# Optimization experiments

Measured on AMD Instinct MI355X. Metric: run time of the kernel, lower is better.

The kernel has to match this reference:

```python
import jax, jax.numpy as jnp
import numpy as np

N, D = 8192, 1024


def setup_inputs() -> dict:
    key = jax.random.key(0)
    k1, k2, k3 = jax.random.split(key, 3)
    f_1 = jax.random.normal(k1, (N, D), dtype=jnp.float32)
    f_2 = jax.random.normal(k2, (N, D), dtype=jnp.float32)
    f_3 = jax.random.normal(k3, (N, D), dtype=jnp.float32)
    return {"f_1": f_1, "f_2": f_2, "f_3": f_3, "batch": 3}


def _svdvals(x):
    # torch.svd computes full U, S, V; only singular values are consumed.
    return jnp.linalg.svd(x, compute_uv=False)


def reference(f_1, f_2, f_3, batch):
    if batch == 2:
        s_1 = _svdvals(f_1)
        if f_2.shape[0] == 0:
            return s_1[0] ** 2
        s_2 = _svdvals(f_2)
        return s_1.mean() + s_2.mean()
    elif batch == 3:
        s_1 = _svdvals(f_1)
        s_2 = _svdvals(f_2)
        s_3 = _svdvals(f_3)
        return s_1[0] ** 2 + 0.5 * (s_2[0] ** 2 + s_3[0] ** 2)
```

## Files before the change

### kernel.cpp

```cpp
#include <hip/hip_runtime.h>


#define DIM 1024
#define NROW 8192
#define MSZ (DIM*DIM)
#define NS 6

typedef __attribute__((ext_vector_type(8))) short short8;
typedef __attribute__((ext_vector_type(4))) float f32x4;

__device__ inline float bf2f(unsigned short u) {
    union { unsigned i; float f; } x; x.i = ((unsigned)u) << 16; return x.f;
}
__device__ inline unsigned short f2bf(float f) {
    union { float f; unsigned i; } x; x.f = f;
    unsigned r = x.i + 0x7FFFu + ((x.i >> 16) & 1u);
    return (unsigned short)(r >> 16);
}
__device__ inline void gload16(const void* g, void* l) {
    __builtin_amdgcn_global_load_lds(
        (const __attribute__((address_space(1))) unsigned int*)g,
        (__attribute__((address_space(3))) unsigned int*)l, 16, 0, 0);
}

__global__ __launch_bounds__(256)
void tconv_k(const float* __restrict__ f0, const float* __restrict__ f1,
             const float* __restrict__ f2, unsigned short* __restrict__ ft) {
    const int m = blockIdx.z;
    const float* f = (m == 0) ? f0 : (m == 1 ? f1 : f2);
    unsigned short* o = ft + (size_t)m * DIM * NROW;
    __shared__ float T[64][68];
    const int c0 = blockIdx.x * 64, r0 = blockIdx.y * 64;
    const int tid = threadIdx.x;
    const int cx = (tid & 15) * 4, ry = tid >> 4;
#pragma unroll
    for (int i = 0; i < 4; ++i) {
        int r = ry + i * 16;
        float4 v = *(const float4*)&f[(size_t)(r0 + r) * DIM + c0 + cx];
        T[cx + 0][r] = v.x;
        T[cx + 1][r] = v.y;
        T[cx + 2][r] = v.z;
        T[cx + 3][r] = v.w;
    }
    __syncthreads();
#pragma unroll
    for (int i = 0; i < 4; ++i) {
        int c = ry + i * 16;
        float4 g = *(const float4*)&T[c][cx];
        ushort4 u;
        u.x = f2bf(g.x); u.y = f2bf(g.y); u.z = f2bf(g.z); u.w = f2bf(g.w);
        *(ushort4*)&o[(size_t)(c0 + c) * NROW + r0 + cx] = u;
    }
}

__global__ __launch_bounds__(256)
void syrk_sk(const unsigned short* __restrict__ src, size_t mstride, int KF,
             float* __restrict__ Gp) {
    const int m = blockIdx.z;
    const unsigned short* S = src + (size_t)m * mstride;
    int idx = blockIdx.x, ti = 0;
    while (idx >= 8 - ti) { idx -= 8 - ti; ++ti; }
    const int tj = ti + idx;
    const int i0 = ti * 128, j0 = tj * 128;
    float* G = Gp + ((size_t)m * 36 + blockIdx.x) * 16384;
    const int Kc = KF / gridDim.y;
    const int k0b = blockIdx.y * Kc;

    __shared__ unsigned short As[2 * 128 * 32];
    __shared__ unsigned short Bs[2 * 128 * 32];

    const int tid = threadIdx.x, w = tid >> 6, lane = tid & 63;
    const int wi = w >> 1, wj = w & 1;

    f32x4 acc[4][4];
#pragma unroll
    for (int a = 0; a < 4; ++a)
#pragma unroll
        for (int b = 0; b < 4; ++b) acc[a][b] = (f32x4){0.f, 0.f, 0.f, 0.f};

    const int lr = lane >> 2;
    const int ksw = (((lane & 3) ^ ((lane >> 4) & 3)) * 8);
    const int fr = lane & 15;
    const int slot = (((lane >> 4) ^ ((fr >> 2) & 3)) * 8);

    for (int k0 = k0b; k0 < k0b + Kc; k0 += 64) {
#pragma unroll
        for (int h = 0; h < 2; ++h)
#pragma unroll
            for (int q = 0; q < 2; ++q) {
                int rr = w * 32 + q * 16;
                gload16(S + (size_t)(i0 + rr + lr) * KF + k0 + h * 32 + ksw,
                        &As[h * 4096 + rr * 32]);
                gload16(S + (size_t)(j0 + rr + lr) * KF + k0 + h * 32 + ksw,
                        &Bs[h * 4096 + rr * 32]);
            }
        __syncthreads();
#pragma unroll
        for (int h = 0; h < 2; ++h) {
            short8 af[4], bfv[4];
#pragma unroll
            for (int a = 0; a < 4; ++a)
                af[a] = *(const short8*)&As[h * 4096 + (wi * 64 + a * 16 + fr) * 32 + slot];
#pragma unroll
            for (int b = 0; b < 4; ++b)
                bfv[b] = *(const short8*)&Bs[h * 4096 + (wj * 64 + b * 16 + fr) * 32 + slot];
#pragma unroll
            for (int a = 0; a < 4; ++a)
#pragma unroll
                for (int b = 0; b < 4; ++b)
                    acc[a][b] = __builtin_amdgcn_mfma_f32_16x16x32_bf16(
                        af[a], bfv[b], acc[a][b], 0, 0, 0);
        }
        __syncthreads();
    }

    const int qr = (lane >> 4) * 4, cn = lane & 15;
#pragma unroll
    for (int a = 0; a < 4; ++a)
#pragma unroll
        for (int b = 0; b < 4; ++b) {
            int cl = wj * 64 + b * 16 + cn;
#pragma unroll
            for (int reg = 0; reg < 4; ++reg) {
                int rl = wi * 64 + a * 16 + qr + reg;
                atomicAdd(&G[rl * 128 + cl], acc[a][b][reg]);
            }
        }
}

__global__ __launch_bounds__(256)
void convert_k(const float* __restrict__ Gp, float* __restrict__ trout,
               unsigned short* __restrict__ dst) {
    const int m = blockIdx.z;
    int idx = blockIdx.x, ti = 0;
    while (idx >= 8 - ti) { idx -= 8 - ti; ++ti; }
    const int tj = ti + idx;
    const int i0 = ti * 128, j0 = tj * 128;
    const float* G = Gp + ((size_t)m * 36 + blockIdx.x) * 16384;
    unsigned short* D = dst + (size_t)m * MSZ;
    __shared__ unsigned short T[128][136];
    const int tid = threadIdx.x;
    const int cx = (tid & 31) * 4, ry = tid >> 5;
    float dtr = 0.f;
#pragma unroll 4
    for (int t = 0; t < 16; ++t) {
        int r = ry + t * 8;
        float4 g = *(const float4*)&G[r * 128 + cx];
        ushort4 o;
        o.x = f2bf(g.x); o.y = f2bf(g.y); o.z = f2bf(g.z); o.w = f2bf(g.w);
        *(ushort4*)&D[(size_t)(i0 + r) * DIM + j0 + cx] = o;
        int rs = r ^ (cx & 124);
        T[cx + 0][rs] = o.x; T[cx + 1][rs] = o.y;
        T[cx + 2][rs] = o.z; T[cx + 3][rs] = o.w;
        if (ti == tj) {
            int d = r - cx;
            if (d >= 0 && d < 4)
                dtr += (d == 0 ? g.x : d == 1 ? g.y : d == 2 ? g.z : g.w);
        }
    }
    if (ti == tj) atomicAdd(&trout[m], dtr);
    if (ti != tj) {
        __syncthreads();
#pragma unroll 4
        for (int t = 0; t < 16; ++t) {
            int p = ry + t * 8;
            int qs = cx ^ (p & 124);
            ushort4 o = *(const ushort4*)&T[p][qs];
            *(ushort4*)&D[(size_t)(j0 + p) * DIM + i0 + cx] = o;
        }
    }
}

__global__ __launch_bounds__(256)
void sq_k(const unsigned short* __restrict__ src, const float* __restrict__ trin,
          float* __restrict__ trout, unsigned short* __restrict__ dst) {
    const int m = blockIdx.z;
    const unsigned short* S = src + (size_t)m * MSZ;
    unsigned short* D = dst + (size_t)m * MSZ;
    int idx = blockIdx.x, ti = 0;
    while (idx >= 16 - ti) { idx -= 16 - ti; ++ti; }
    const int tj = ti + idx;
    const int i0 = ti * 64, j0 = tj * 64;
    float tv = trin[m];
    const float sc = 1.f / (tv * tv);

    __shared__ unsigned short As[2 * 64 * 32];
    __shared__ unsigned short Bs[2 * 64 * 32];
    __shared__ unsigned short Ts[64][68];

    const int tid = threadIdx.x, w = tid >> 6, lane = tid & 63;
    const int wi = w >> 1, wj = w & 1;
    f32x4 acc[2][2];
#pragma unroll
    for (int a = 0; a < 2; ++a)
#pragma unroll
        for (int b = 0; b < 2; ++b) acc[a][b] = (f32x4){0.f, 0.f, 0.f, 0.f};

    const int lr = lane >> 2;
    const int ksw = (((lane & 3) ^ ((lane >> 4) & 3)) * 8);
    const int fr = lane & 15;
    const int slot = (((lane >> 4) ^ ((fr >> 2) & 3)) * 8);

    for (int k0 = 0; k0 < DIM; k0 += 64) {
#pragma unroll
        for (int h = 0; h < 2; ++h) {
            gload16(S + (size_t)(i0 + w * 16 + lr) * DIM + k0 + h * 32 + ksw,
                    &As[h * 2048 + w * 16 * 32]);
            gload16(S + (size_t)(j0 + w * 16 + lr) * DIM + k0 + h * 32 + ksw,
                    &Bs[h * 2048 + w * 16 * 32]);
        }
        __syncthreads();
#pragma unroll
        for (int h = 0; h < 2; ++h) {
            short8 af[2], bfv[2];
#pragma unroll
            for (int a = 0; a < 2; ++a)
                af[a] = *(const short8*)&As[h * 2048 + (wi * 32 + a * 16 + fr) * 32 + slot];
#pragma unroll
            for (int c = 0; c < 2; ++c)
                bfv[c] = *(const short8*)&Bs[h * 2048 + (wj * 32 + c * 16 + fr) * 32 + slot];
#pragma unroll
            for (int a = 0; a < 2; ++a)
#pragma unroll
                for (int c = 0; c < 2; ++c)
                    acc[a][c] = __builtin_amdgcn_mfma_f32_16x16x32_bf16(
                        af[a], bfv[c], acc[a][c], 0, 0, 0);
        }
        __syncthreads();
    }

    const int qr = (lane >> 4) * 4, cn = lane & 15;
#pragma unroll
    for (int a = 0; a < 2; ++a)
#pragma unroll
        for (int b = 0; b < 2; ++b) {
            int cl = wj * 32 + b * 16 + cn;
#pragma unroll
            for (int reg = 0; reg < 4; ++reg) {
                int rl = wi * 32 + a * 16 + qr + reg;
                unsigned short val = f2bf(acc[a][b][reg] * sc);
                D[(size_t)(i0 + rl) * DIM + j0 + cl] = val;
                Ts[cl][rl] = val;
            }
        }
    if (ti == tj && wi == wj) {
        int d = cn - qr;
        if (d >= 0 && d < 4)
            atomicAdd(&trout[m], (acc[0][0][d] + acc[1][1][d]) * sc);
    }
    if (ti != tj) {
        __syncthreads();
        const int cx = (tid & 15) * 4, ry = tid >> 4;
#pragma unroll
        for (int tq = 0; tq < 4; ++tq) {
            int p = ry + tq * 16;
            ushort4 o;
            o.x = Ts[p][cx + 0]; o.y = Ts[p][cx + 1];
            o.z = Ts[p][cx + 2]; o.w = Ts[p][cx + 3];
            *(ushort4*)&D[(size_t)(j0 + p) * DIM + i0 + cx] = o;
        }
    }
}

__global__ __launch_bounds__(256)
void mv_bf16(const unsigned short* __restrict__ M, const float* __restrict__ vin,
             float* __restrict__ vout) {
    int m = blockIdx.y;
    const unsigned short* A = M + (size_t)m * MSZ;
    int wv = threadIdx.x >> 6, lane = threadIdx.x & 63;
    int row = blockIdx.x * 4 + wv;
    const unsigned short* a = A + (size_t)row * DIM;
    float s = 0.f;
    if (vin) {
        const float* v = vin + m * DIM;
        for (int j = lane; j < DIM; j += 64) s += bf2f(a[j]) * v[j];
    } else {
        for (int j = lane; j < DIM; j += 64) s += bf2f(a[j]);
    }
    for (int off = 32; off; off >>= 1) s += __shfl_down(s, off);
    if (lane == 0) vout[m * DIM + row] = s;
}

__global__ __launch_bounds__(256)
void ray_k(const float* __restrict__ Gp, const float* __restrict__ wv,
           float* __restrict__ num) {
    const int m = blockIdx.y;
    int idx = blockIdx.x, ti = 0;
    while (idx >= 8 - ti) { idx -= 8 - ti; ++ti; }
    const int tj = ti + idx;
    const float* G = Gp + ((size_t)m * 36 + blockIdx.x) * 16384;
    const float* wi = wv + m * DIM + ti * 128;
    const float* wj = wv + m * DIM + tj * 128;
    const int tid = threadIdx.x;
    const int r = tid >> 1, c0 = (tid & 1) * 64;
    float inner = 0.f;
    const float4* g4 = (const float4*)&G[r * 128 + c0];
    const float4* w4 = (const float4*)&wj[c0];
#pragma unroll
    for (int t = 0; t < 16; ++t) {
        float4 g = g4[t], ww = w4[t];
        inner += g.x * ww.x + g.y * ww.y + g.z * ww.z + g.w * ww.w;
    }
    float s = wi[r] * inner;
    for (int off = 32; off; off >>= 1) s += __shfl_down(s, off);
    __shared__ float part[4];
    int lane = tid & 63, wx = tid >> 6;
    if (lane == 0) part[wx] = s;
    __syncthreads();
    if (tid == 0) {
        float tot = part[0] + part[1] + part[2] + part[3];
        if (ti != tj) tot *= 2.f;
        atomicAdd(&num[m], tot);
    }
}

__global__ __launch_bounds__(256)
void final_k(const float* __restrict__ num, const float* __restrict__ w,
             float* __restrict__ out) {
    __shared__ float red[256];
    int tid = threadIdx.x;
    float lam[3];
    for (int m = 0; m < 3; ++m) {
        float s = 0.f;
        for (int i = tid; i < DIM; i += 256) { float x = w[m * DIM + i]; s += x * x; }
        red[tid] = s; __syncthreads();
        for (int off = 128; off; off >>= 1) {
            if (tid < off) red[tid] += red[tid + off];
            __syncthreads();
        }
        lam[m] = num[m] / red[0]; __syncthreads();
    }
    if (tid == 0) out[0] = lam[0] + 0.5f * (lam[1] + lam[2]);
}

extern "C" void kernel_launch(void* const* d_in, const int* in_sizes, int n_in,
                              void* d_out, int out_size, void* d_ws, size_t ws_size,
                              hipStream_t stream) {
    const float* f0 = (const float*)d_in[0];
    const float* f1 = (const float*)d_in[1];
    const float* f2 = (const float*)d_in[2];

    char* base = (char*)d_ws;
    unsigned short* ft = (unsigned short*)base;
    unsigned short* Q  = (unsigned short*)base;
    unsigned short* P  = (unsigned short*)(base + 50331648);
    float* G32 = (float*)(base + 56623104);
    float* trbuf = (float*)(base + 63700992);
    float* num = trbuf + 40;
    float* v = (float*)(base + 63701248);
    float* w = v + 3 * DIM;

    hipMemsetAsync(G32, 0, 7078144, stream);

    dim3 gt(DIM / 64, NROW / 64, 3);
    tconv_k<<<gt, 256, 0, stream>>>(f0, f1, f2, ft);

    syrk_sk<<<dim3(36, 4, 3), 256, 0, stream>>>(ft, (size_t)DIM * NROW, NROW, G32);
    convert_k<<<dim3(36, 1, 3), 256, 0, stream>>>(G32, trbuf, P);

    unsigned short* cur = P;
    unsigned short* nxt = Q;
    for (int s = 0; s < NS; ++s) {
        sq_k<<<dim3(136, 1, 3), 256, 0, stream>>>(cur, trbuf + s * 3,
                                                  trbuf + (s + 1) * 3, nxt);
        unsigned short* t2 = cur; cur = nxt; nxt = t2;
    }

    dim3 b(256, 1, 1);
    dim3 gm(DIM / 4, 3, 1);
    mv_bf16<<<gm, b, 0, stream>>>(cur, nullptr, v);
    mv_bf16<<<gm, b, 0, stream>>>(cur, v, w);

    ray_k<<<dim3(36, 3, 1), 256, 0, stream>>>(G32, w, num);
    final_k<<<1, 256, 0, stream>>>(num, w, (float*)d_out);
}
```

Baseline: 312.2 us.

## Fuse six squaring launches into one persistent kernel with a grid barrier

Replaces the six per-step launches of the matrix-squaring kernel with a single persistent kernel. It loops over the steps internally, ping-ponging between P and Q, and synchronises all 408 blocks through an atomic-counter grid barrier. The aim is to remove kernel launch gaps and tail effects between dependent steps. The cost is a spin-wait barrier that relies on all blocks being co-resident, and each step then finishes at the pace of the slowest block.

After: 580.0 us. 1.86x slower.

```diff
diff --git a/kernel.cpp b/kernel.cpp
--- a/kernel.cpp
+++ b/kernel.cpp
@@ -5,6 +5,7 @@
 #define NROW 8192
 #define MSZ (DIM*DIM)
 #define NS 6
+#define NBLK 408
 
 typedef __attribute__((ext_vector_type(8))) short short8;
 typedef __attribute__((ext_vector_type(4))) float f32x4;
@@ -172,17 +173,13 @@
 }
 
 __global__ __launch_bounds__(256)
-void sq_k(const unsigned short* __restrict__ src, const float* __restrict__ trin,
-          float* __restrict__ trout, unsigned short* __restrict__ dst) {
-    const int m = blockIdx.z;
-    const unsigned short* S = src + (size_t)m * MSZ;
-    unsigned short* D = dst + (size_t)m * MSZ;
+void chain_k(unsigned short* __restrict__ P, unsigned short* __restrict__ Q,
+             float* __restrict__ trbuf, unsigned int* __restrict__ bar) {
+    const int m = blockIdx.y;
     int idx = blockIdx.x, ti = 0;
     while (idx >= 16 - ti) { idx -= 16 - ti; ++ti; }
     const int tj = ti + idx;
     const int i0 = ti * 64, j0 = tj * 64;
-    float tv = trin[m];
-    const float sc = 1.f / (tv * tv);
 
     __shared__ unsigned short As[2 * 64 * 32];
     __shared__ unsigned short Bs[2 * 64 * 32];
@@ -190,75 +187,94 @@
 
     const int tid = threadIdx.x, w = tid >> 6, lane = tid & 63;
     const int wi = w >> 1, wj = w & 1;
-    f32x4 acc[2][2];
-#pragma unroll
-    for (int a = 0; a < 2; ++a)
-#pragma unroll
-        for (int b = 0; b < 2; ++b) acc[a][b] = (f32x4){0.f, 0.f, 0.f, 0.f};
-
     const int lr = lane >> 2;
     const int ksw = (((lane & 3) ^ ((lane >> 4) & 3)) * 8);
     const int fr = lane & 15;
     const int slot = (((lane >> 4) ^ ((fr >> 2) & 3)) * 8);
-
-    for (int k0 = 0; k0 < DIM; k0 += 64) {
-#pragma unroll
-        for (int h = 0; h < 2; ++h) {
-            gload16(S + (size_t)(i0 + w * 16 + lr) * DIM + k0 + h * 32 + ksw,
-                    &As[h * 2048 + w * 16 * 32]);
-            gload16(S + (size_t)(j0 + w * 16 + lr) * DIM + k0 + h * 32 + ksw,
-                    &Bs[h * 2048 + w * 16 * 32]);
-        }
-        __syncthreads();
-#pragma unroll
-        for (int h = 0; h < 2; ++h) {
-            short8 af[2], bfv[2];
-#pragma unroll
-            for (int a = 0; a < 2; ++a)
-                af[a] = *(const short8*)&As[h * 2048 + (wi * 32 + a * 16 + fr) * 32 + slot];
-#pragma unroll
-            for (int c = 0; c < 2; ++c)
-                bfv[c] = *(const short8*)&Bs[h * 2048 + (wj * 32 + c * 16 + fr) * 32 + slot];
-#pragma unroll
-            for (int a = 0; a < 2; ++a)
+    const int qr = (lane >> 4) * 4, cn = lane & 15;
+
+    for (int s = 0; s < NS; ++s) {
+        const unsigned short* S = ((s & 1) ? Q : P) + (size_t)m * MSZ;
+        unsigned short* D = ((s & 1) ? P : Q) + (size_t)m * MSZ;
+        float tv = trbuf[s * 3 + m];
+        const float sc = 1.f / (tv * tv);
+
+        f32x4 acc[2][2];
+#pragma unroll
+        for (int a = 0; a < 2; ++a)
+#pragma unroll
+            for (int b = 0; b < 2; ++b) acc[a][b] = (f32x4){0.f, 0.f, 0.f, 0.f};
+
+        for (int k0 = 0; k0 < DIM; k0 += 64) {
+#pragma unroll
+            for (int h = 0; h < 2; ++h) {
+                gload16(S + (size_t)(i0 + w * 16 + lr) * DIM + k0 + h * 32 + ksw,
+                        &As[h * 2048 + w * 16 * 32]);
+                gload16(S + (size_t)(j0 + w * 16 + lr) * DIM + k0 + h * 32 + ksw,
+                        &Bs[h * 2048 + w * 16 * 32]);
+            }
+            __syncthreads();
+#pragma unroll
+            for (int h = 0; h < 2; ++h) {
+                short8 af[2], bfv[2];
+#pragma unroll
+                for (int a = 0; a < 2; ++a)
+                    af[a] = *(const short8*)&As[h * 2048 + (wi * 32 + a * 16 + fr) * 32 + slot];
 #pragma unroll
                 for (int c = 0; c < 2; ++c)
-                    acc[a][c] = __builtin_amdgcn_mfma_f32_16x16x32_bf16(
-                        af[a], bfv[c], acc[a][c], 0, 0, 0);
-        }
-        __syncthreads();
-    }
-
-    const int qr = (lane >> 4) * 4, cn = lane & 15;
-#pragma unroll
-    for (int a = 0; a < 2; ++a)
-#pragma unroll
-        for (int b = 0; b < 2; ++b) {
-            int cl = wj * 32 + b * 16 + cn;
-#pragma unroll
-            for (int reg = 0; reg < 4; ++reg) {
-                int rl = wi * 32 + a * 16 + qr + reg;
-                unsigned short val = f2bf(acc[a][b][reg] * sc);
-                D[(size_t)(i0 + rl) * DIM + j0 + cl] = val;
-                Ts[cl][rl] = val;
-            }
-        }
-    if (ti == tj && wi == wj) {
-        int d = cn - qr;
-        if (d >= 0 && d < 4)
-            atomicAdd(&trout[m], (acc[0][0][d] + acc[1][1][d]) * sc);
-    }
-    if (ti != tj) {
-        __syncthreads();
-        const int cx = (tid & 15) * 4, ry = tid >> 4;
-#pragma unroll
-        for (int tq = 0; tq < 4; ++tq) {
-            int p = ry + tq * 16;
-            ushort4 o;
-            o.x = Ts[p][cx + 0]; o.y = Ts[p][cx + 1];
-            o.z = Ts[p][cx + 2]; o.w = Ts[p][cx + 3];
-            *(ushort4*)&D[(size_t)(j0 + p) * DIM + i0 + cx] = o;
-        }
+                    bfv[c] = *(const short8*)&Bs[h * 2048 + (wj * 32 + c * 16 + fr) * 32 + slot];
+#pragma unroll
+                for (int a = 0; a < 2; ++a)
+#pragma unroll
+                    for (int c = 0; c < 2; ++c)
+                        acc[a][c] = __builtin_amdgcn_mfma_f32_16x16x32_bf16(
+                            af[a], bfv[c], acc[a][c], 0, 0, 0);
+            }
+            __syncthreads();
+        }
+
+#pragma unroll
+        for (int a = 0; a < 2; ++a)
+#pragma unroll
+            for (int b = 0; b < 2; ++b) {
+                int cl = wj * 32 + b * 16 + cn;
+#pragma unroll
+                for (int reg = 0; reg < 4; ++reg) {
+                    int rl = wi * 32 + a * 16 + qr + reg;
+                    unsigned short val = f2bf(acc[a][b][reg] * sc);
+                    D[(size_t)(i0 + rl) * DIM + j0 + cl] = val;
+                    Ts[cl][rl] = val;
+                }
+            }
+        if (ti == tj && wi == wj) {
+            int d = cn - qr;
+            if (d >= 0 && d < 4)
+                atomicAdd(&trbuf[(s + 1) * 3 + m],
+                          (acc[0][0][d] + acc[1][1][d]) * sc);
+        }
+        if (ti != tj) {
+            __syncthreads();
+            const int cx = (tid & 15) * 4, ry = tid >> 4;
+#pragma unroll
+            for (int tq = 0; tq < 4; ++tq) {
+                int p = ry + tq * 16;
+                ushort4 o;
+                o.x = Ts[p][cx + 0]; o.y = Ts[p][cx + 1];
+                o.z = Ts[p][cx + 2]; o.w = Ts[p][cx + 3];
+                *(ushort4*)&D[(size_t)(j0 + p) * DIM + i0 + cx] = o;
+            }
+        }
+
+        __syncthreads();
+        if (tid == 0) {
+            __threadfence();
+            atomicAdd(bar, 1u);
+            unsigned int target = (unsigned int)(s + 1) * NBLK;
+            while (atomicAdd(bar, 0u) < target)
+                __builtin_amdgcn_s_sleep(8);
+            __threadfence();
+        }
+        __syncthreads();
     }
 }
 
@@ -347,6 +363,7 @@
     float* G32 = (float*)(base + 56623104);
     float* trbuf = (float*)(base + 63700992);
     float* num = trbuf + 40;
+    unsigned int* bar = (unsigned int*)(trbuf + 48);
     float* v = (float*)(base + 63701248);
     float* w = v + 3 * DIM;
 
@@ -358,18 +375,12 @@
     syrk_sk<<<dim3(36, 4, 3), 256, 0, stream>>>(ft, (size_t)DIM * NROW, NROW, G32);
     convert_k<<<dim3(36, 1, 3), 256, 0, stream>>>(G32, trbuf, P);
 
-    unsigned short* cur = P;
-    unsigned short* nxt = Q;
-    for (int s = 0; s < NS; ++s) {
-        sq_k<<<dim3(136, 1, 3), 256, 0, stream>>>(cur, trbuf + s * 3,
-                                                  trbuf + (s + 1) * 3, nxt);
-        unsigned short* t2 = cur; cur = nxt; nxt = t2;
-    }
+    chain_k<<<dim3(136, 3, 1), 256, 0, stream>>>(P, Q, trbuf, bar);
 
     dim3 b(256, 1, 1);
     dim3 gm(DIM / 4, 3, 1);
-    mv_bf16<<<gm, b, 0, stream>>>(cur, nullptr, v);
-    mv_bf16<<<gm, b, 0, stream>>>(cur, v, w);
+    mv_bf16<<<gm, b, 0, stream>>>(P, nullptr, v);
+    mv_bf16<<<gm, b, 0, stream>>>(P, v, w);
 
     ray_k<<<dim3(36, 3, 1), 256, 0, stream>>>(G32, w, num);
     final_k<<<1, 256, 0, stream>>>(num, w, (float*)d_out);
```
